# Kernel tuning notes

Hardware: AMD Instinct MI355X
Metric: run time of the kernel (lower is better)

## Reference

```python
import jax, jax.numpy as jnp
import numpy as np

EPS = 1e-5


def _batchnorm(x, gamma, beta):
    # training-mode batch norm over the node axis, per feature channel
    mean = jnp.mean(x, axis=0)
    var = jnp.var(x, axis=0)  # biased variance, as torch uses for normalization
    return (x - mean) * jax.lax.rsqrt(var + EPS) * gamma + beta


def _gcn_conv(h, W, b, src, dst, norm, n_nodes):
    # h: [N, Fin] -> [N, Fout]; D^{-1/2}(A+I)D^{-1/2} (h W) + b
    h = h @ W                                   # [N, Fout]
    msgs = h[src] * norm[:, None]               # [E+N, Fout] gathered, normalized
    out = jax.ops.segment_sum(msgs, dst, num_segments=n_nodes)
    return out + b


def setup_inputs() -> dict:
    key = jax.random.key(0)
    ks = jax.random.split(key, 8)
    N, F, E, H = 50000, 512, 800000, 256
    inp = {
        "x": jax.random.normal(ks[0], (N, F), jnp.float32),
        "edge_index": jax.random.randint(ks[1], (2, E), 0, N, jnp.int64),
        "gamma1": jnp.ones((F,), jnp.float32),
        "beta1": jnp.zeros((F,), jnp.float32),
        "W1": jax.random.normal(ks[2], (F, H), jnp.float32) * (1.0 / np.sqrt(F)),
        "b1": jnp.zeros((H,), jnp.float32),
        "W2": jax.random.normal(ks[3], (H, H), jnp.float32) * (1.0 / np.sqrt(H)),
        "b2": jnp.zeros((H,), jnp.float32),
        "W3": jax.random.normal(ks[4], (H, H), jnp.float32) * (1.0 / np.sqrt(H)),
        "b3": jnp.zeros((H,), jnp.float32),
        "W4": jax.random.normal(ks[5], (H, H), jnp.float32) * (1.0 / np.sqrt(H)),
        "b4": jnp.zeros((H,), jnp.float32),
        "gamma2": jnp.ones((H,), jnp.float32),
        "beta2": jnp.zeros((H,), jnp.float32),
        "Wd": jax.random.normal(ks[6], (H, 5), jnp.float32) * (1.0 / np.sqrt(H)),
        "bd": jnp.zeros((5,), jnp.float32),
    }
    return inp


def reference(x, edge_index, gamma1, beta1, W1, b1, W2, b2, W3, b3, W4, b4,
              gamma2, beta2, Wd, bd):
    N = x.shape[0]
    loops = jnp.arange(N, dtype=edge_index.dtype)
    src = jnp.concatenate([edge_index[0], loops])
    dst = jnp.concatenate([edge_index[1], loops])
    deg = jax.ops.segment_sum(jnp.ones_like(src, dtype=x.dtype), dst, num_segments=N)
    dinv = jax.lax.rsqrt(deg)                    # deg >= 1 due to self-loops
    norm = dinv[src] * dinv[dst]                 # [E+N]

    h = _batchnorm(x, gamma1, beta1)
    h = _gcn_conv(h, W1, b1, src, dst, norm, N)
    h = _gcn_conv(h, W2, b2, src, dst, norm, N)
    h = _gcn_conv(h, W3, b3, src, dst, norm, N)
    h = _gcn_conv(h, W4, b4, src, dst, norm, N)
    h = _batchnorm(h, gamma2, beta2)
    # Flatten(start_dim=1) is identity on [N, 256]
    return jax.nn.sigmoid(h @ Wd + bd)           # [N, 5]
```

## Files before the change

kernel.cpp:

```cpp
#include <hip/hip_runtime.h>
#include <math.h>

#define BN_EPS 1e-5f

typedef float floatx4 __attribute__((ext_vector_type(4)));
typedef short shortx4 __attribute__((ext_vector_type(4)));
typedef short shortx8 __attribute__((ext_vector_type(8)));
typedef __bf16 bf16x8 __attribute__((ext_vector_type(8)));

__device__ __forceinline__ unsigned short f2b(float f) {
    unsigned int u = __builtin_bit_cast(unsigned int, f);
    u += 0x7fffu + ((u >> 16) & 1u);
    return (unsigned short)(u >> 16);
}
__device__ __forceinline__ float b2f(unsigned short s) {
    unsigned int u = ((unsigned int)s) << 16;
    return __builtin_bit_cast(float, u);
}
__device__ __forceinline__ float b2f_s(short s) { return b2f((unsigned short)s); }

__global__ __launch_bounds__(256)
void k_detect(const unsigned int* __restrict__ ei, int n_check, int* __restrict__ flag) {
    __shared__ int any;
    if (threadIdx.x == 0) any = 0;
    __syncthreads();
    for (int i = threadIdx.x; i < n_check; i += 256) {
        if (ei[2 * i + 1] != 0u) any = 1;
    }
    __syncthreads();
    if (threadIdx.x == 0) *flag = any;
}

__global__ __launch_bounds__(256)
void k_count(const void* __restrict__ ei_raw, const int* __restrict__ flag,
             int* __restrict__ cnt, int E) {
    int e = blockIdx.x * 256 + threadIdx.x;
    if (e >= E) return;
    int d = (*flag) ? ((const int*)ei_raw)[E + e]
                    : (int)((const long long*)ei_raw)[E + e];
    atomicAdd(&cnt[d], 1);
}

__global__ __launch_bounds__(1024)
void k_scan_sum(const int* __restrict__ cnt, int* __restrict__ bsum, int N) {
    __shared__ int s[1024];
    int i = blockIdx.x * 1024 + threadIdx.x;
    s[threadIdx.x] = (i < N) ? cnt[i] : 0;
    __syncthreads();
    for (int off = 512; off > 0; off >>= 1) {
        if (threadIdx.x < off) s[threadIdx.x] += s[threadIdx.x + off];
        __syncthreads();
    }
    if (threadIdx.x == 0) bsum[blockIdx.x] = s[0];
}

__global__ __launch_bounds__(1024)
void k_scan_part(int* __restrict__ bsum, int nb) {
    __shared__ int s[1024];
    int t = threadIdx.x;
    int v = (t < nb) ? bsum[t] : 0;
    s[t] = v;
    __syncthreads();
    for (int off = 1; off < 1024; off <<= 1) {
        int tmp = (t >= off) ? s[t - off] : 0;
        __syncthreads();
        s[t] += tmp;
        __syncthreads();
    }
    if (t < nb) bsum[t] = s[t] - v;
}

__global__ __launch_bounds__(1024)
void k_scan_final(const int* __restrict__ cnt, const int* __restrict__ bsum,
                  int* __restrict__ row_ptr, int* __restrict__ cursor,
                  float* __restrict__ dinv, int N) {
    __shared__ int s[1024];
    int b = blockIdx.x, t = threadIdx.x;
    int i = b * 1024 + t;
    int v = (i < N) ? cnt[i] : 0;
    s[t] = v;
    __syncthreads();
    for (int off = 1; off < 1024; off <<= 1) {
        int tmp = (t >= off) ? s[t - off] : 0;
        __syncthreads();
        s[t] += tmp;
        __syncthreads();
    }
    if (i < N) {
        int excl = bsum[b] + s[t] - v;
        row_ptr[i] = excl;
        cursor[i]  = excl;
        dinv[i] = rsqrtf((float)(v + 1));
        if (i == N - 1) row_ptr[N] = excl + v;
    }
}

__global__ __launch_bounds__(256)
void k_fill(const void* __restrict__ ei_raw, const int* __restrict__ flag,
            int* __restrict__ cursor, const float* __restrict__ dinv,
            int2* __restrict__ csr_sw, int E) {
    int e = blockIdx.x * 256 + threadIdx.x;
    if (e >= E) return;
    int s, d;
    if (*flag) {
        const int* a = (const int*)ei_raw;
        s = a[e]; d = a[E + e];
    } else {
        const long long* a = (const long long*)ei_raw;
        s = (int)a[e]; d = (int)a[E + e];
    }
    int p = atomicAdd(&cursor[d], 1);
    float w = dinv[s] * dinv[d];
    csr_sw[p] = make_int2(s, __builtin_bit_cast(int, w));
}

__global__ __launch_bounds__(256)
void k_bnstats_cast(const float* __restrict__ x, unsigned short* __restrict__ xb,
                    float* __restrict__ sum8, float* __restrict__ sumsq8, int N, int F) {
    __shared__ float ls[512], lq[512];
    int q   = F >> 2;
    int t   = threadIdx.x;
    int cq  = t % q;
    int ro  = t / q;
    int rpp = 256 / q;
    int step = gridDim.x * rpp;
    float s0 = 0.f, s1 = 0.f, s2 = 0.f, s3 = 0.f;
    float q0 = 0.f, q1 = 0.f, q2 = 0.f, q3 = 0.f;
    size_t colb = (size_t)cq * 4;
    for (int r = blockIdx.x * rpp + ro; r < N; r += 4 * step) {
        int rb = r + step, rc = r + 2 * step, rd = r + 3 * step;
        bool ob = rb < N, oc = rc < N, od = rd < N;
        float4 va = *(const float4*)&x[(size_t)r * F + colb];
        float4 vb, vc, vd;
        if (ob) vb = *(const float4*)&x[(size_t)rb * F + colb];
        if (oc) vc = *(const float4*)&x[(size_t)rc * F + colb];
        if (od) vd = *(const float4*)&x[(size_t)rd * F + colb];
        shortx4 o;
        o[0] = (short)f2b(va.x); o[1] = (short)f2b(va.y);
        o[2] = (short)f2b(va.z); o[3] = (short)f2b(va.w);
        *(shortx4*)&xb[(size_t)r * F + colb] = o;
        s0 += va.x; s1 += va.y; s2 += va.z; s3 += va.w;
        q0 += va.x * va.x; q1 += va.y * va.y; q2 += va.z * va.z; q3 += va.w * va.w;
        if (ob) {
            o[0] = (short)f2b(vb.x); o[1] = (short)f2b(vb.y);
            o[2] = (short)f2b(vb.z); o[3] = (short)f2b(vb.w);
            *(shortx4*)&xb[(size_t)rb * F + colb] = o;
            s0 += vb.x; s1 += vb.y; s2 += vb.z; s3 += vb.w;
            q0 += vb.x * vb.x; q1 += vb.y * vb.y; q2 += vb.z * vb.z; q3 += vb.w * vb.w;
        }
        if (oc) {
            o[0] = (short)f2b(vc.x); o[1] = (short)f2b(vc.y);
            o[2] = (short)f2b(vc.z); o[3] = (short)f2b(vc.w);
            *(shortx4*)&xb[(size_t)rc * F + colb] = o;
            s0 += vc.x; s1 += vc.y; s2 += vc.z; s3 += vc.w;
            q0 += vc.x * vc.x; q1 += vc.y * vc.y; q2 += vc.z * vc.z; q3 += vc.w * vc.w;
        }
        if (od) {
            o[0] = (short)f2b(vd.x); o[1] = (short)f2b(vd.y);
            o[2] = (short)f2b(vd.z); o[3] = (short)f2b(vd.w);
            *(shortx4*)&xb[(size_t)rd * F + colb] = o;
            s0 += vd.x; s1 += vd.y; s2 += vd.z; s3 += vd.w;
            q0 += vd.x * vd.x; q1 += vd.y * vd.y; q2 += vd.z * vd.z; q3 += vd.w * vd.w;
        }
    }
    for (int c = t; c < F; c += 256) { ls[c] = 0.f; lq[c] = 0.f; }
    __syncthreads();
    atomicAdd(&ls[cq * 4 + 0], s0); atomicAdd(&ls[cq * 4 + 1], s1);
    atomicAdd(&ls[cq * 4 + 2], s2); atomicAdd(&ls[cq * 4 + 3], s3);
    atomicAdd(&lq[cq * 4 + 0], q0); atomicAdd(&lq[cq * 4 + 1], q1);
    atomicAdd(&lq[cq * 4 + 2], q2); atomicAdd(&lq[cq * 4 + 3], q3);
    __syncthreads();
    int rep = (blockIdx.x & 7) * F;
    for (int c = t; c < F; c += 256) {
        atomicAdd(&sum8[rep + c],   ls[c]);
        atomicAdd(&sumsq8[rep + c], lq[c]);
    }
}

__global__ __launch_bounds__(256)
void k_bnstats_b(const unsigned short* __restrict__ x, float* __restrict__ sum,
                 float* __restrict__ sumsq, int N, int H) {
    __shared__ float ls[256], lq[256];
    int t  = threadIdx.x;
    int cg = t & 31;
    int ro = t >> 5;
    int step = gridDim.x * 8;
    float s[8], q[8];
    #pragma unroll
    for (int j = 0; j < 8; ++j) { s[j] = 0.f; q[j] = 0.f; }
    for (int r = blockIdx.x * 8 + ro; r < N; r += step) {
        shortx8 v = *(const shortx8*)&x[(size_t)r * H + cg * 8];
        #pragma unroll
        for (int j = 0; j < 8; ++j) {
            float f = b2f_s(v[j]);
            s[j] += f; q[j] += f * f;
        }
    }
    ls[t] = 0.f; lq[t] = 0.f;
    __syncthreads();
    #pragma unroll
    for (int j = 0; j < 8; ++j) {
        atomicAdd(&ls[cg * 8 + j], s[j]);
        atomicAdd(&lq[cg * 8 + j], q[j]);
    }
    __syncthreads();
    int rep = (blockIdx.x & 3) * H;
    atomicAdd(&sum[rep + t],   ls[t]);
    atomicAdd(&sumsq[rep + t], lq[t]);
}

__global__ __launch_bounds__(256)
void k_bnfin(const float* __restrict__ sum, const float* __restrict__ sumsq,
             const float* __restrict__ gamma, const float* __restrict__ beta,
             float* __restrict__ a, float* __restrict__ b, int N, int F, int nrep) {
    int c = blockIdx.x * 256 + threadIdx.x;
    if (c >= F) return;
    float s = 0.f, ss = 0.f;
    for (int i = 0; i < nrep; ++i) { s += sum[i * F + c]; ss += sumsq[i * F + c]; }
    float m   = s / (float)N;
    float var = ss / (float)N - m * m;
    float rs  = rsqrtf(var + BN_EPS);
    float aa  = gamma[c] * rs;
    a[c] = aa;
    b[c] = beta[c] - m * aa;
}

__global__ __launch_bounds__(256)
void k_prep_w(const float* __restrict__ W1, const float* __restrict__ W2,
              const float* __restrict__ W3, const float* __restrict__ W4,
              unsigned short* __restrict__ T1, unsigned short* __restrict__ T2,
              unsigned short* __restrict__ T3, unsigned short* __restrict__ T4,
              const float* __restrict__ bna, const float* __restrict__ bnb,
              float* __restrict__ cvec, int F, int H, int wblocks) {
    if ((int)blockIdx.x >= wblocks) {
        int bi = blockIdx.x - wblocks;
        int j = threadIdx.x;
        int kslice = F / 8;
        int k0 = bi * kslice;
        float s = 0.f;
        for (int k = k0; k < k0 + kslice; ++k)
            s += bnb[k] * W1[(size_t)k * H + j];
        atomicAdd(&cvec[j], s);
        return;
    }
    int i = blockIdx.x * 256 + threadIdx.x;
    int n1 = F * H, n2 = H * H;
    if (i < n1) {
        int n = i / F, k = i % F;
        T1[i] = f2b(W1[(size_t)k * H + n] * bna[k]);
        return;
    }
    const float* W; unsigned short* T; int j;
    if (i < n1 + n2)          { W = W2; T = T2; j = i - n1; }
    else if (i < n1 + 2 * n2) { W = W3; T = T3; j = i - n1 - n2; }
    else if (i < n1 + 3 * n2) { W = W4; T = T4; j = i - n1 - 2 * n2; }
    else return;
    int n = j / H, k = j % H;
    T[j] = f2b(W[(size_t)k * H + n]);
}

__device__ __forceinline__ void glds16(const void* g, void* l) {
    __builtin_amdgcn_global_load_lds(
        (const __attribute__((address_space(1))) unsigned int*)g,
        (__attribute__((address_space(3))) unsigned int*)l, 16, 0, 0);
}

__global__ __launch_bounds__(256)
void k_gemm_bf16(const unsigned short* __restrict__ A, const unsigned short* __restrict__ Bt,
                 unsigned short* __restrict__ C, int K, int NC) {
    __shared__ unsigned short As[128 * 32];
    __shared__ unsigned short Bs[128 * 32];
    int tid  = threadIdx.x;
    int wave = tid >> 6, lane = tid & 63;
    int row0 = blockIdx.x * 128;
    int col0 = blockIdx.y * 128;
    int wr = (wave & 1) * 64;
    int wc = (wave >> 1) * 64;

    floatx4 acc[4][4];
    #pragma unroll
    for (int i = 0; i < 4; i++)
        #pragma unroll
        for (int j = 0; j < 4; j++) acc[i][j] = (floatx4){0.f, 0.f, 0.f, 0.f};

    int cA = tid * 16;
    int cB = cA + 4096;
    const char* Ab = (const char*)A;
    const char* Bb = (const char*)Bt;
    size_t a_off0 = (size_t)(row0 + (cA >> 6)) * K * 2 + (cA & 63);
    size_t a_off1 = (size_t)(row0 + (cB >> 6)) * K * 2 + (cB & 63);
    size_t b_off0 = (size_t)(col0 + (cA >> 6)) * K * 2 + (cA & 63);
    size_t b_off1 = (size_t)(col0 + (cB >> 6)) * K * 2 + (cB & 63);

    int lm  = lane & 15;
    int lk8 = (lane >> 4) * 8;

    for (int ks = 0; ks < K; ks += 32) {
        size_t koff = (size_t)ks * 2;
        glds16(Ab + a_off0 + koff, (char*)As + cA);
        glds16(Ab + a_off1 + koff, (char*)As + cA + 4096);
        glds16(Bb + b_off0 + koff, (char*)Bs + cA);
        glds16(Bb + b_off1 + koff, (char*)Bs + cA + 4096);
        __syncthreads();

        bf16x8 af[4], bfr[4];
        #pragma unroll
        for (int i = 0; i < 4; i++) {
            shortx8 s = *(const shortx8*)&As[(wr + i * 16 + lm) * 32 + lk8];
            af[i] = __builtin_bit_cast(bf16x8, s);
        }
        #pragma unroll
        for (int j = 0; j < 4; j++) {
            shortx8 s = *(const shortx8*)&Bs[(wc + j * 16 + lm) * 32 + lk8];
            bfr[j] = __builtin_bit_cast(bf16x8, s);
        }
        #pragma unroll
        for (int i = 0; i < 4; i++)
            #pragma unroll
            for (int j = 0; j < 4; j++)
                acc[i][j] = __builtin_amdgcn_mfma_f32_16x16x32_bf16(bfr[j], af[i], acc[i][j], 0, 0, 0);
        __syncthreads();
    }

    int quad = lane >> 4;
    int crow0 = row0 + wr + lm;
    int ccol0 = col0 + wc + quad * 4;
    #pragma unroll
    for (int i = 0; i < 4; i++) {
        size_t rbase = (size_t)(crow0 + i * 16) * NC;
        #pragma unroll
        for (int j = 0; j < 4; j++) {
            shortx4 o;
            o[0] = (short)f2b(acc[i][j][0]);
            o[1] = (short)f2b(acc[i][j][1]);
            o[2] = (short)f2b(acc[i][j][2]);
            o[3] = (short)f2b(acc[i][j][3]);
            *(shortx4*)&C[rbase + ccol0 + j * 16] = o;
        }
    }
}

__global__ __launch_bounds__(256)
void k_agg(const unsigned short* __restrict__ hin, unsigned short* __restrict__ hout,
           const int* __restrict__ row_ptr, const int2* __restrict__ csr_sw,
           const float* __restrict__ dinv, const float* __restrict__ bias, int N) {
    const int H = 256;
    int node = blockIdx.x * 4 + (threadIdx.x >> 6);
    if (node >= N) return;
    int lane = threadIdx.x & 63;
    int half = lane >> 5;
    int f = (lane & 31) * 8;
    float acc[8];
    float di = dinv[node];
    if (half == 0) {
        shortx8 hv = *(const shortx8*)&hin[(size_t)node * H + f];
        float sl = di * di;
        #pragma unroll
        for (int j = 0; j < 8; ++j) acc[j] = b2f_s(hv[j]) * sl;
    } else {
        #pragma unroll
        for (int j = 0; j < 8; ++j) acc[j] = 0.f;
    }
    int e0 = row_ptr[node], e1 = row_ptr[node + 1];
    int e = e0;
    for (; e + 8 <= e1; e += 8) {
        int2 p0 = csr_sw[e + 0 + half];
        int2 p1 = csr_sw[e + 2 + half];
        int2 p2 = csr_sw[e + 4 + half];
        int2 p3 = csr_sw[e + 6 + half];
        shortx8 r0 = *(const shortx8*)&hin[(size_t)p0.x * H + f];
        shortx8 r1 = *(const shortx8*)&hin[(size_t)p1.x * H + f];
        shortx8 r2 = *(const shortx8*)&hin[(size_t)p2.x * H + f];
        shortx8 r3 = *(const shortx8*)&hin[(size_t)p3.x * H + f];
        float w0 = __builtin_bit_cast(float, p0.y);
        float w1 = __builtin_bit_cast(float, p1.y);
        float w2 = __builtin_bit_cast(float, p2.y);
        float w3 = __builtin_bit_cast(float, p3.y);
        #pragma unroll
        for (int j = 0; j < 8; ++j)
            acc[j] += w0 * b2f_s(r0[j]) + w1 * b2f_s(r1[j])
                    + w2 * b2f_s(r2[j]) + w3 * b2f_s(r3[j]);
    }
    for (; e < e1; e += 2) {
        int idx = e + half;
        bool valid = idx < e1;
        int2 pr = csr_sw[valid ? idx : e];
        float w = valid ? __builtin_bit_cast(float, pr.y) : 0.f;
        shortx8 r = *(const shortx8*)&hin[(size_t)pr.x * H + f];
        #pragma unroll
        for (int j = 0; j < 8; ++j) acc[j] += w * b2f_s(r[j]);
    }
    #pragma unroll
    for (int j = 0; j < 8; ++j) acc[j] += __shfl_xor(acc[j], 32, 64);
    if (half == 0) {
        float4 bi0 = *(const float4*)&bias[f];
        float4 bi1 = *(const float4*)&bias[f + 4];
        shortx8 o;
        o[0] = (short)f2b(acc[0] + bi0.x);
        o[1] = (short)f2b(acc[1] + bi0.y);
        o[2] = (short)f2b(acc[2] + bi0.z);
        o[3] = (short)f2b(acc[3] + bi0.w);
        o[4] = (short)f2b(acc[4] + bi1.x);
        o[5] = (short)f2b(acc[5] + bi1.y);
        o[6] = (short)f2b(acc[6] + bi1.z);
        o[7] = (short)f2b(acc[7] + bi1.w);
        *(shortx8*)&hout[(size_t)node * H + f] = o;
    }
}

__global__ __launch_bounds__(256)
void k_agg_c(const unsigned short* __restrict__ hin, unsigned short* __restrict__ hout,
             const int* __restrict__ row_ptr, const int2* __restrict__ csr_sw,
             const float* __restrict__ dinv, const float* __restrict__ bias,
             const float* __restrict__ cvec, int N) {
    const int H = 256;
    int node = blockIdx.x * 4 + (threadIdx.x >> 6);
    if (node >= N) return;
    int lane = threadIdx.x & 63;
    int half = lane >> 5;
    int f = (lane & 31) * 8;
    float acc[8];
    float ws;
    float di = dinv[node];
    if (half == 0) {
        shortx8 hv = *(const shortx8*)&hin[(size_t)node * H + f];
        float sl = di * di;
        ws = sl;
        #pragma unroll
        for (int j = 0; j < 8; ++j) acc[j] = b2f_s(hv[j]) * sl;
    } else {
        ws = 0.f;
        #pragma unroll
        for (int j = 0; j < 8; ++j) acc[j] = 0.f;
    }
    int e0 = row_ptr[node], e1 = row_ptr[node + 1];
    int e = e0;
    for (; e + 8 <= e1; e += 8) {
        int2 p0 = csr_sw[e + 0 + half];
        int2 p1 = csr_sw[e + 2 + half];
        int2 p2 = csr_sw[e + 4 + half];
        int2 p3 = csr_sw[e + 6 + half];
        shortx8 r0 = *(const shortx8*)&hin[(size_t)p0.x * H + f];
        shortx8 r1 = *(const shortx8*)&hin[(size_t)p1.x * H + f];
        shortx8 r2 = *(const shortx8*)&hin[(size_t)p2.x * H + f];
        shortx8 r3 = *(const shortx8*)&hin[(size_t)p3.x * H + f];
        float w0 = __builtin_bit_cast(float, p0.y);
        float w1 = __builtin_bit_cast(float, p1.y);
        float w2 = __builtin_bit_cast(float, p2.y);
        float w3 = __builtin_bit_cast(float, p3.y);
        ws += (w0 + w1) + (w2 + w3);
        #pragma unroll
        for (int j = 0; j < 8; ++j)
            acc[j] += w0 * b2f_s(r0[j]) + w1 * b2f_s(r1[j])
                    + w2 * b2f_s(r2[j]) + w3 * b2f_s(r3[j]);
    }
    for (; e < e1; e += 2) {
        int idx = e + half;
        bool valid = idx < e1;
        int2 pr = csr_sw[valid ? idx : e];
        float w = valid ? __builtin_bit_cast(float, pr.y) : 0.f;
        shortx8 r = *(const shortx8*)&hin[(size_t)pr.x * H + f];
        ws += w;
        #pragma unroll
        for (int j = 0; j < 8; ++j) acc[j] += w * b2f_s(r[j]);
    }
    #pragma unroll
    for (int j = 0; j < 8; ++j) acc[j] += __shfl_xor(acc[j], 32, 64);
    ws += __shfl_xor(ws, 32, 64);
    if (half == 0) {
        float4 bi0 = *(const float4*)&bias[f];
        float4 bi1 = *(const float4*)&bias[f + 4];
        float4 c0 = *(const float4*)&cvec[f];
        float4 c1 = *(const float4*)&cvec[f + 4];
        bi0.x += ws * c0.x; bi0.y += ws * c0.y;
        bi0.z += ws * c0.z; bi0.w += ws * c0.w;
        bi1.x += ws * c1.x; bi1.y += ws * c1.y;
        bi1.z += ws * c1.z; bi1.w += ws * c1.w;
        shortx8 o;
        o[0] = (short)f2b(acc[0] + bi0.x);
        o[1] = (short)f2b(acc[1] + bi0.y);
        o[2] = (short)f2b(acc[2] + bi0.z);
        o[3] = (short)f2b(acc[3] + bi0.w);
        o[4] = (short)f2b(acc[4] + bi1.x);
        o[5] = (short)f2b(acc[5] + bi1.y);
        o[6] = (short)f2b(acc[6] + bi1.z);
        o[7] = (short)f2b(acc[7] + bi1.w);
        *(shortx8*)&hout[(size_t)node * H + f] = o;
    }
}

__global__ __launch_bounds__(256)
void k_head(const unsigned short* __restrict__ h, const float* __restrict__ a,
            const float* __restrict__ b, const float* __restrict__ Wd,
            const float* __restrict__ bd, float* __restrict__ out, int N) {
    int node = blockIdx.x * 4 + (threadIdx.x >> 6);
    if (node >= N) return;
    int lane = threadIdx.x & 63;
    int f = lane * 4;
    shortx4 hv = *(const shortx4*)&h[(size_t)node * 256 + f];
    float v0 = b2f_s(hv[0]) * a[f + 0] + b[f + 0];
    float v1 = b2f_s(hv[1]) * a[f + 1] + b[f + 1];
    float v2 = b2f_s(hv[2]) * a[f + 2] + b[f + 2];
    float v3 = b2f_s(hv[3]) * a[f + 3] + b[f + 3];
    float s[5];
    #pragma unroll
    for (int j = 0; j < 5; ++j) {
        s[j] = v0 * Wd[(f + 0) * 5 + j] + v1 * Wd[(f + 1) * 5 + j] +
               v2 * Wd[(f + 2) * 5 + j] + v3 * Wd[(f + 3) * 5 + j];
    }
    #pragma unroll
    for (int off = 32; off > 0; off >>= 1) {
        #pragma unroll
        for (int j = 0; j < 5; ++j) s[j] += __shfl_down(s[j], off, 64);
    }
    if (lane == 0) {
        #pragma unroll
        for (int j = 0; j < 5; ++j) {
            float z = s[j] + bd[j];
            out[(size_t)node * 5 + j] = 1.f / (1.f + expf(-z));
        }
    }
}

extern "C" void kernel_launch(void* const* d_in, const int* in_sizes, int n_in,
                              void* d_out, int out_size, void* d_ws, size_t ws_size,
                              hipStream_t stream) {
    const float* x      = (const float*)d_in[0];
    const void*  ei_raw = d_in[1];
    const float* gamma1 = (const float*)d_in[2];
    const float* beta1  = (const float*)d_in[3];
    const float* W1 = (const float*)d_in[4];
    const float* b1 = (const float*)d_in[5];
    const float* W2 = (const float*)d_in[6];
    const float* b2 = (const float*)d_in[7];
    const float* W3 = (const float*)d_in[8];
    const float* b3 = (const float*)d_in[9];
    const float* W4 = (const float*)d_in[10];
    const float* b4 = (const float*)d_in[11];
    const float* gamma2 = (const float*)d_in[12];
    const float* beta2  = (const float*)d_in[13];
    const float* Wd = (const float*)d_in[14];
    const float* bd = (const float*)d_in[15];

    const int F = in_sizes[2];
    const int N = in_sizes[0] / F;
    const int E = in_sizes[1] / 2;
    const int H = in_sizes[5];
    const int Mpad = ((N + 127) / 128) * 128;
    const int NB   = (N + 1023) / 1024;
    float* out = (float*)d_out;

    char* p = (char*)d_ws;
    auto alloc = [&](size_t bytes) {
        void* r = (void*)p;
        p += (bytes + 255) & ~(size_t)255;
        return r;
    };
    int*   flag    = (int*)  alloc(4);
    char*  zstart  = p;
    int*   cnt     = (int*)  alloc((size_t)N * 4);
    float* colsum8 = (float*)alloc((size_t)8 * F * 4);
    float* colsq8  = (float*)alloc((size_t)8 * F * 4);
    float* colsum2 = (float*)alloc((size_t)4 * H * 4);
    float* colsq2  = (float*)alloc((size_t)4 * H * 4);
    float* cvec    = (float*)alloc((size_t)H * 4);
    size_t zbytes  = (size_t)(p - zstart);
    int*   row_ptr = (int*)  alloc(((size_t)N + 1) * 4);
    int*   cursor  = (int*)  alloc((size_t)N * 4);
    float* dinv    = (float*)alloc((size_t)N * 4);
    int2*  csr_sw  = (int2*) alloc((size_t)E * 8);
    int*   bsum    = (int*)  alloc((size_t)NB * 4);
    float* bna     = (float*)alloc((size_t)F * 4);
    float* bnb     = (float*)alloc((size_t)F * 4);
    unsigned short* W1t = (unsigned short*)alloc((size_t)F * H * 2);
    unsigned short* W2t = (unsigned short*)alloc((size_t)H * H * 2);
    unsigned short* W3t = (unsigned short*)alloc((size_t)H * H * 2);
    unsigned short* W4t = (unsigned short*)alloc((size_t)H * H * 2);
    unsigned short* xb  = (unsigned short*)alloc((size_t)Mpad * F * 2);
    unsigned short* hbA = (unsigned short*)alloc((size_t)Mpad * H * 2);
    unsigned short* hbB = (unsigned short*)alloc((size_t)Mpad * H * 2);

    hipMemsetAsync(zstart, 0, zbytes, stream);
    hipMemsetAsync(xb + (size_t)N * F, 0, (size_t)(Mpad - N) * F * 2, stream);

    int n_check = (E >= 2048) ? 2048 : E;
    k_detect<<<1, 256, 0, stream>>>((const unsigned int*)ei_raw, n_check, flag);
    k_count<<<(E + 255) / 256, 256, 0, stream>>>(ei_raw, flag, cnt, E);
    k_scan_sum<<<NB, 1024, 0, stream>>>(cnt, bsum, N);
    k_scan_part<<<1, 1024, 0, stream>>>(bsum, NB);
    k_scan_final<<<NB, 1024, 0, stream>>>(cnt, bsum, row_ptr, cursor, dinv, N);
    k_fill<<<(E + 255) / 256, 256, 0, stream>>>(ei_raw, flag, cursor, dinv, csr_sw, E);

    k_bnstats_cast<<<2048, 256, 0, stream>>>(x, xb, colsum8, colsq8, N, F);
    k_bnfin<<<(F + 255) / 256, 256, 0, stream>>>(colsum8, colsq8, gamma1, beta1, bna, bnb, N, F, 8);

    int tot = F * H + 3 * H * H;
    int wblocks = (tot + 255) / 256;
    k_prep_w<<<wblocks + 8, 256, 0, stream>>>(W1, W2, W3, W4, W1t, W2t, W3t, W4t,
                                              bna, bnb, cvec, F, H, wblocks);

    dim3 gg(Mpad / 128, H / 128);
    int aggb = (N + 3) / 4;
    k_gemm_bf16<<<gg, 256, 0, stream>>>(xb, W1t, hbA, F, H);
    k_agg_c<<<aggb, 256, 0, stream>>>(hbA, hbB, row_ptr, csr_sw, dinv, b1, cvec, N);
    k_gemm_bf16<<<gg, 256, 0, stream>>>(hbB, W2t, hbA, H, H);
    k_agg<<<aggb, 256, 0, stream>>>(hbA, hbB, row_ptr, csr_sw, dinv, b2, N);
    k_gemm_bf16<<<gg, 256, 0, stream>>>(hbB, W3t, hbA, H, H);
    k_agg<<<aggb, 256, 0, stream>>>(hbA, hbB, row_ptr, csr_sw, dinv, b3, N);
    k_gemm_bf16<<<gg, 256, 0, stream>>>(hbB, W4t, hbA, H, H);
    k_agg<<<aggb, 256, 0, stream>>>(hbA, hbB, row_ptr, csr_sw, dinv, b4, N);

    k_bnstats_b<<<1024, 256, 0, stream>>>(hbB, colsum2, colsq2, N, H);
    k_bnfin<<<(H + 255) / 256, 256, 0, stream>>>(colsum2, colsq2, gamma2, beta2, bna, bnb, N, H, 4);
    k_head<<<(N + 3) / 4, 256, 0, stream>>>(hbB, bna, bnb, Wd, bd, out, N);
}
```

Measured before the change: 709.3 us.

## Record atomic slot in count pass, drop second atomic pass; use native bf16 cast

The count kernel now saves each edge's atomic return value, so CSR placement computes its slot as row_ptr[dst]+seq with no second round of atomics on a cursor array. The float-to-bf16 conversion moves from manual bit rounding to the compiler's native __bf16 cast, which may map to a hardware convert instruction. The BN-stats/cast kernel is reorganised so each thread handles 8 contiguous columns per row and writes 16-byte stores. The price is an extra E-sized int array written and then read back.

```diff
diff --git a/kernel.cpp b/kernel.cpp
--- a/kernel.cpp
+++ b/kernel.cpp
@@ -8,16 +8,13 @@
 typedef short shortx8 __attribute__((ext_vector_type(8)));
 typedef __bf16 bf16x8 __attribute__((ext_vector_type(8)));
 
-__device__ __forceinline__ unsigned short f2b(float f) {
-    unsigned int u = __builtin_bit_cast(unsigned int, f);
-    u += 0x7fffu + ((u >> 16) & 1u);
-    return (unsigned short)(u >> 16);
-}
-__device__ __forceinline__ float b2f(unsigned short s) {
-    unsigned int u = ((unsigned int)s) << 16;
+__device__ __forceinline__ short f2bs(float f) {
+    return __builtin_bit_cast(short, (__bf16)f);
+}
+__device__ __forceinline__ float b2f_s(short s) {
+    unsigned int u = ((unsigned int)(unsigned short)s) << 16;
     return __builtin_bit_cast(float, u);
 }
-__device__ __forceinline__ float b2f_s(short s) { return b2f((unsigned short)s); }
 
 __global__ __launch_bounds__(256)
 void k_detect(const unsigned int* __restrict__ ei, int n_check, int* __restrict__ flag) {
@@ -32,13 +29,13 @@
 }
 
 __global__ __launch_bounds__(256)
-void k_count(const void* __restrict__ ei_raw, const int* __restrict__ flag,
-             int* __restrict__ cnt, int E) {
+void k_count_seq(const void* __restrict__ ei_raw, const int* __restrict__ flag,
+                 int* __restrict__ cnt, int* __restrict__ seq, int E) {
     int e = blockIdx.x * 256 + threadIdx.x;
     if (e >= E) return;
     int d = (*flag) ? ((const int*)ei_raw)[E + e]
                     : (int)((const long long*)ei_raw)[E + e];
-    atomicAdd(&cnt[d], 1);
+    seq[e] = atomicAdd(&cnt[d], 1);
 }
 
 __global__ __launch_bounds__(1024)
@@ -72,8 +69,7 @@
 
 __global__ __launch_bounds__(1024)
 void k_scan_final(const int* __restrict__ cnt, const int* __restrict__ bsum,
-                  int* __restrict__ row_ptr, int* __restrict__ cursor,
-                  float* __restrict__ dinv, int N) {
+                  int* __restrict__ row_ptr, float* __restrict__ dinv, int N) {
     __shared__ int s[1024];
     int b = blockIdx.x, t = threadIdx.x;
     int i = b * 1024 + t;
@@ -89,16 +85,15 @@
     if (i < N) {
         int excl = bsum[b] + s[t] - v;
         row_ptr[i] = excl;
-        cursor[i]  = excl;
         dinv[i] = rsqrtf((float)(v + 1));
         if (i == N - 1) row_ptr[N] = excl + v;
     }
 }
 
 __global__ __launch_bounds__(256)
-void k_fill(const void* __restrict__ ei_raw, const int* __restrict__ flag,
-            int* __restrict__ cursor, const float* __restrict__ dinv,
-            int2* __restrict__ csr_sw, int E) {
+void k_place(const void* __restrict__ ei_raw, const int* __restrict__ flag,
+             const int* __restrict__ row_ptr, const int* __restrict__ seq,
+             const float* __restrict__ dinv, int2* __restrict__ csr_sw, int E) {
     int e = blockIdx.x * 256 + threadIdx.x;
     if (e >= E) return;
     int s, d;
@@ -109,7 +104,7 @@
         const long long* a = (const long long*)ei_raw;
         s = (int)a[e]; d = (int)a[E + e];
     }
-    int p = atomicAdd(&cursor[d], 1);
+    int p = row_ptr[d] + seq[e];
     float w = dinv[s] * dinv[d];
     csr_sw[p] = make_int2(s, __builtin_bit_cast(int, w));
 }
@@ -118,57 +113,33 @@
 void k_bnstats_cast(const float* __restrict__ x, unsigned short* __restrict__ xb,
                     float* __restrict__ sum8, float* __restrict__ sumsq8, int N, int F) {
     __shared__ float ls[512], lq[512];
-    int q   = F >> 2;
-    int t   = threadIdx.x;
-    int cq  = t % q;
-    int ro  = t / q;
-    int rpp = 256 / q;
-    int step = gridDim.x * rpp;
-    float s0 = 0.f, s1 = 0.f, s2 = 0.f, s3 = 0.f;
-    float q0 = 0.f, q1 = 0.f, q2 = 0.f, q3 = 0.f;
-    size_t colb = (size_t)cq * 4;
-    for (int r = blockIdx.x * rpp + ro; r < N; r += 4 * step) {
-        int rb = r + step, rc = r + 2 * step, rd = r + 3 * step;
-        bool ob = rb < N, oc = rc < N, od = rd < N;
-        float4 va = *(const float4*)&x[(size_t)r * F + colb];
-        float4 vb, vc, vd;
-        if (ob) vb = *(const float4*)&x[(size_t)rb * F + colb];
-        if (oc) vc = *(const float4*)&x[(size_t)rc * F + colb];
-        if (od) vd = *(const float4*)&x[(size_t)rd * F + colb];
-        shortx4 o;
-        o[0] = (short)f2b(va.x); o[1] = (short)f2b(va.y);
-        o[2] = (short)f2b(va.z); o[3] = (short)f2b(va.w);
-        *(shortx4*)&xb[(size_t)r * F + colb] = o;
-        s0 += va.x; s1 += va.y; s2 += va.z; s3 += va.w;
-        q0 += va.x * va.x; q1 += va.y * va.y; q2 += va.z * va.z; q3 += va.w * va.w;
-        if (ob) {
-            o[0] = (short)f2b(vb.x); o[1] = (short)f2b(vb.y);
-            o[2] = (short)f2b(vb.z); o[3] = (short)f2b(vb.w);
-            *(shortx4*)&xb[(size_t)rb * F + colb] = o;
-            s0 += vb.x; s1 += vb.y; s2 += vb.z; s3 += vb.w;
-            q0 += vb.x * vb.x; q1 += vb.y * vb.y; q2 += vb.z * vb.z; q3 += vb.w * vb.w;
-        }
-        if (oc) {
-            o[0] = (short)f2b(vc.x); o[1] = (short)f2b(vc.y);
-            o[2] = (short)f2b(vc.z); o[3] = (short)f2b(vc.w);
-            *(shortx4*)&xb[(size_t)rc * F + colb] = o;
-            s0 += vc.x; s1 += vc.y; s2 += vc.z; s3 += vc.w;
-            q0 += vc.x * vc.x; q1 += vc.y * vc.y; q2 += vc.z * vc.z; q3 += vc.w * vc.w;
-        }
-        if (od) {
-            o[0] = (short)f2b(vd.x); o[1] = (short)f2b(vd.y);
-            o[2] = (short)f2b(vd.z); o[3] = (short)f2b(vd.w);
-            *(shortx4*)&xb[(size_t)rd * F + colb] = o;
-            s0 += vd.x; s1 += vd.y; s2 += vd.z; s3 += vd.w;
-            q0 += vd.x * vd.x; q1 += vd.y * vd.y; q2 += vd.z * vd.z; q3 += vd.w * vd.w;
-        }
-    }
-    for (int c = t; c < F; c += 256) { ls[c] = 0.f; lq[c] = 0.f; }
-    __syncthreads();
-    atomicAdd(&ls[cq * 4 + 0], s0); atomicAdd(&ls[cq * 4 + 1], s1);
-    atomicAdd(&ls[cq * 4 + 2], s2); atomicAdd(&ls[cq * 4 + 3], s3);
-    atomicAdd(&lq[cq * 4 + 0], q0); atomicAdd(&lq[cq * 4 + 1], q1);
-    atomicAdd(&lq[cq * 4 + 2], q2); atomicAdd(&lq[cq * 4 + 3], q3);
+    int t  = threadIdx.x;
+    int cg = t & 63;
+    int ro = t >> 6;
+    int step = gridDim.x * 4;
+    float s[8], q[8];
+    #pragma unroll
+    for (int j = 0; j < 8; ++j) { s[j] = 0.f; q[j] = 0.f; }
+    size_t colb = (size_t)cg * 8;
+    for (int r = blockIdx.x * 4 + ro; r < N; r += step) {
+        float4 v0 = *(const float4*)&x[(size_t)r * F + colb];
+        float4 v1 = *(const float4*)&x[(size_t)r * F + colb + 4];
+        shortx8 o;
+        o[0] = f2bs(v0.x); o[1] = f2bs(v0.y); o[2] = f2bs(v0.z); o[3] = f2bs(v0.w);
+        o[4] = f2bs(v1.x); o[5] = f2bs(v1.y); o[6] = f2bs(v1.z); o[7] = f2bs(v1.w);
+        *(shortx8*)&xb[(size_t)r * F + colb] = o;
+        s[0] += v0.x; s[1] += v0.y; s[2] += v0.z; s[3] += v0.w;
+        s[4] += v1.x; s[5] += v1.y; s[6] += v1.z; s[7] += v1.w;
+        q[0] += v0.x * v0.x; q[1] += v0.y * v0.y; q[2] += v0.z * v0.z; q[3] += v0.w * v0.w;
+        q[4] += v1.x * v1.x; q[5] += v1.y * v1.y; q[6] += v1.z * v1.z; q[7] += v1.w * v1.w;
+    }
+    ls[t] = 0.f; lq[t] = 0.f; ls[t + 256] = 0.f; lq[t + 256] = 0.f;
+    __syncthreads();
+    #pragma unroll
+    for (int j = 0; j < 8; ++j) {
+        atomicAdd(&ls[cg * 8 + j], s[j]);
+        atomicAdd(&lq[cg * 8 + j], q[j]);
+    }
     __syncthreads();
     int rep = (blockIdx.x & 7) * F;
     for (int c = t; c < F; c += 256) {
@@ -247,7 +218,7 @@
     int n1 = F * H, n2 = H * H;
     if (i < n1) {
         int n = i / F, k = i % F;
-        T1[i] = f2b(W1[(size_t)k * H + n] * bna[k]);
+        T1[i] = (unsigned short)f2bs(W1[(size_t)k * H + n] * bna[k]);
         return;
     }
     const float* W; unsigned short* T; int j;
@@ -256,7 +227,7 @@
     else if (i < n1 + 3 * n2) { W = W4; T = T4; j = i - n1 - 2 * n2; }
     else return;
     int n = j / H, k = j % H;
-    T[j] = f2b(W[(size_t)k * H + n]);
+    T[j] = (unsigned short)f2bs(W[(size_t)k * H + n]);
 }
 
 __device__ __forceinline__ void glds16(const void* g, void* l) {
@@ -331,10 +302,10 @@
         #pragma unroll
         for (int j = 0; j < 4; j++) {
             shortx4 o;
-            o[0] = (short)f2b(acc[i][j][0]);
-            o[1] = (short)f2b(acc[i][j][1]);
-            o[2] = (short)f2b(acc[i][j][2]);
-            o[3] = (short)f2b(acc[i][j][3]);
+            o[0] = f2bs(acc[i][j][0]);
+            o[1] = f2bs(acc[i][j][1]);
+            o[2] = f2bs(acc[i][j][2]);
+            o[3] = f2bs(acc[i][j][3]);
             *(shortx4*)&C[rbase + ccol0 + j * 16] = o;
         }
     }
@@ -396,14 +367,14 @@
         float4 bi0 = *(const float4*)&bias[f];
         float4 bi1 = *(const float4*)&bias[f + 4];
         shortx8 o;
-        o[0] = (short)f2b(acc[0] + bi0.x);
-        o[1] = (short)f2b(acc[1] + bi0.y);
-        o[2] = (short)f2b(acc[2] + bi0.z);
-        o[3] = (short)f2b(acc[3] + bi0.w);
-        o[4] = (short)f2b(acc[4] + bi1.x);
-        o[5] = (short)f2b(acc[5] + bi1.y);
-        o[6] = (short)f2b(acc[6] + bi1.z);
-        o[7] = (short)f2b(acc[7] + bi1.w);
+        o[0] = f2bs(acc[0] + bi0.x);
+        o[1] = f2bs(acc[1] + bi0.y);
+        o[2] = f2bs(acc[2] + bi0.z);
+        o[3] = f2bs(acc[3] + bi0.w);
+        o[4] = f2bs(acc[4] + bi1.x);
+        o[5] = f2bs(acc[5] + bi1.y);
+        o[6] = f2bs(acc[6] + bi1.z);
+        o[7] = f2bs(acc[7] + bi1.w);
         *(shortx8*)&hout[(size_t)node * H + f] = o;
     }
 }
@@ -477,14 +448,14 @@
         bi1.x += ws * c1.x; bi1.y += ws * c1.y;
         bi1.z += ws * c1.z; bi1.w += ws * c1.w;
         shortx8 o;
-        o[0] = (short)f2b(acc[0] + bi0.x);
-        o[1] = (short)f2b(acc[1] + bi0.y);
-        o[2] = (short)f2b(acc[2] + bi0.z);
-        o[3] = (short)f2b(acc[3] + bi0.w);
-        o[4] = (short)f2b(acc[4] + bi1.x);
-        o[5] = (short)f2b(acc[5] + bi1.y);
-        o[6] = (short)f2b(acc[6] + bi1.z);
-        o[7] = (short)f2b(acc[7] + bi1.w);
+        o[0] = f2bs(acc[0] + bi0.x);
+        o[1] = f2bs(acc[1] + bi0.y);
+        o[2] = f2bs(acc[2] + bi0.z);
+        o[3] = f2bs(acc[3] + bi0.w);
+        o[4] = f2bs(acc[4] + bi1.x);
+        o[5] = f2bs(acc[5] + bi1.y);
+        o[6] = f2bs(acc[6] + bi1.z);
+        o[7] = f2bs(acc[7] + bi1.w);
         *(shortx8*)&hout[(size_t)node * H + f] = o;
     }
 }
@@ -566,7 +537,7 @@
     float* cvec    = (float*)alloc((size_t)H * 4);
     size_t zbytes  = (size_t)(p - zstart);
     int*   row_ptr = (int*)  alloc(((size_t)N + 1) * 4);
-    int*   cursor  = (int*)  alloc((size_t)N * 4);
+    int*   seq     = (int*)  alloc((size_t)E * 4);
     float* dinv    = (float*)alloc((size_t)N * 4);
     int2*  csr_sw  = (int2*) alloc((size_t)E * 8);
     int*   bsum    = (int*)  alloc((size_t)NB * 4);
@@ -585,11 +556,11 @@
 
     int n_check = (E >= 2048) ? 2048 : E;
     k_detect<<<1, 256, 0, stream>>>((const unsigned int*)ei_raw, n_check, flag);
-    k_count<<<(E + 255) / 256, 256, 0, stream>>>(ei_raw, flag, cnt, E);
+    k_count_seq<<<(E + 255) / 256, 256, 0, stream>>>(ei_raw, flag, cnt, seq, E);
     k_scan_sum<<<NB, 1024, 0, stream>>>(cnt, bsum, N);
     k_scan_part<<<1, 1024, 0, stream>>>(bsum, NB);
-    k_scan_final<<<NB, 1024, 0, stream>>>(cnt, bsum, row_ptr, cursor, dinv, N);
-    k_fill<<<(E + 255) / 256, 256, 0, stream>>>(ei_raw, flag, cursor, dinv, csr_sw, E);
+    k_scan_final<<<NB, 1024, 0, stream>>>(cnt, bsum, row_ptr, dinv, N);
+    k_place<<<(E + 255) / 256, 256, 0, stream>>>(ei_raw, flag, row_ptr, seq, dinv, csr_sw, E);
 
     k_bnstats_cast<<<2048, 256, 0, stream>>>(x, xb, colsum8, colsq8, N, F);
     k_bnfin<<<(F + 255) / 256, 256, 0, stream>>>(colsum8, colsq8, gamma1, beta1, bna, bnb, N, F, 8);
```

Measured after the change: 702.4 us. Within noise of the previous version (-1.0%).
